# Optimization experiments

Hardware: AMD Instinct MI355X
Metric: run time of the kernel (lower is better)

The kernel has to match this reference:

```python
import jax, jax.numpy as jnp
import numpy as np
from jax import lax

# Fixed-point scales (powers of two, as in linger's luna/venus pipeline).
# scale_gi = input_scale * weight_ih_scale, scale_gh = hidden_scale * weight_hh_scale.
SCALE_GI = 2.0 ** 14
SCALE_GH = 2.0 ** 14
Q27 = 2.0 ** 27
Q15 = 2.0 ** 15
Q31 = 2.0 ** 31
INT32_MIN = -(2.0 ** 31)
INT32_MAX = 2.0 ** 31 - 1


def quant_round(x, scale):
    # QuantMode.floor_add: floor(x*scale + 0.5)/scale, with straight-through gradient
    # (linger QAT rounding uses STE).
    q = jnp.floor(x * scale + 0.5) / scale
    return x + lax.stop_gradient(q - x)


@jax.custom_vjp
def qsigmoid(x):
    # Quantize input to Q27 int32, evaluate sigmoid, output Q31 -> requant to Q15.
    i_q27 = jnp.clip(jnp.floor(x * Q27 + 0.5), INT32_MIN, INT32_MAX)
    s = jax.nn.sigmoid(i_q27 / Q27)
    out_q31 = jnp.floor(s * Q31 + 0.5)
    out_q15 = jnp.floor(out_q31 * (2.0 ** -16) + 0.5)  # luna_requant(31 -> 15)
    return out_q15 / Q15

def _qsig_fwd(x):
    return qsigmoid(x), x

def _qsig_bwd(x, g):
    s = jax.nn.sigmoid(x)
    return (g * s * (1.0 - s),)

qsigmoid.defvjp(_qsig_fwd, _qsig_bwd)


@jax.custom_vjp
def qtanh(x):
    i_q27 = jnp.clip(jnp.floor(x * Q27 + 0.5), INT32_MIN, INT32_MAX)
    t = jnp.tanh(i_q27 / Q27)
    out_q31 = jnp.floor(t * Q31 + 0.5)
    out_q15 = jnp.floor(out_q31 * (2.0 ** -16) + 0.5)
    return out_q15 / Q15

def _qtanh_fwd(x):
    return qtanh(x), x

def _qtanh_bwd(x, g):
    t = jnp.tanh(x)
    return (g * (1.0 - t * t),)

qtanh.defvjp(_qtanh_fwd, _qtanh_bwd)


def setup_inputs() -> dict:
    key = jax.random.key(0)
    k = jax.random.split(key, 6)
    B, I, H = 8192, 512, 512
    return {
        "input_x": jax.random.normal(k[0], (B, I), dtype=jnp.float32),
        "hidden": jax.random.normal(k[1], (B, H), dtype=jnp.float32),
        "weight_ih": jax.random.normal(k[2], (3 * H, I), dtype=jnp.float32) * 0.05,
        "weight_hh": jax.random.normal(k[3], (3 * H, H), dtype=jnp.float32) * 0.05,
        "bias_ih": jax.random.normal(k[4], (3 * H,), dtype=jnp.float32) * 0.05,
        "bias_hh": jax.random.normal(k[5], (3 * H,), dtype=jnp.float32) * 0.05,
    }


def reference(input_x, hidden, weight_ih, weight_hh, bias_ih, bias_hh):
    # Dense gate projections: [B, 3H]
    gi = input_x @ weight_ih.T + bias_ih
    gh = hidden @ weight_hh.T + bias_hh
    # Requant gate pre-activations to fixed-point grid (biasih/biashh quantizers)
    gi = quant_round(gi, SCALE_GI)
    gh = quant_round(gh, SCALE_GH)
    i_r, i_i, i_n = jnp.split(gi, 3, axis=1)
    h_r, h_i, h_n = jnp.split(gh, 3, axis=1)
    resetgate = qsigmoid(i_r + h_r)
    inputgate = qsigmoid(i_i + h_i)
    # h_n requantized to Q27, reset*h_n product requantized to Q15
    h_n = quant_round(h_n, Q27)
    resetgate_h_n = quant_round(resetgate * h_n, Q15)
    newgate = qtanh(resetgate_h_n + i_n)
    new_hidden = quant_round(hidden, Q15)
    hy = newgate + inputgate * (new_hidden - newgate)
    return hy
```

## Files before the change

kernel.cpp:

```cpp
#include <hip/hip_runtime.h>
#include <math.h>


typedef _Float16 f16x8  __attribute__((ext_vector_type(8)));
typedef _Float16 f16x4  __attribute__((ext_vector_type(4)));
typedef __bf16   bf16x8 __attribute__((ext_vector_type(8)));
typedef float    f32x16 __attribute__((ext_vector_type(16)));

namespace {

constexpr int Bsz = 8192, Ksz = 512, Hsz = 512;
constexpr int BM = 64, BN = 64;

constexpr unsigned WCH0    = 16384u;
constexpr unsigned NCHUNK  = 16384u + 3072u;
constexpr unsigned WS_F16  = NCHUNK * 512u;
constexpr size_t   WS_NEED = (size_t)WS_F16 * 2;

__device__ __forceinline__ float qround(float x, float s, float invs) {
    return floorf(x * s + 0.5f) * invs;
}

__device__ __forceinline__ float qsigmoid_dev(float x) {
    float iq = floorf(x * 134217728.0f + 0.5f);
    iq = fminf(fmaxf(iq, -2147483648.0f), 2147483648.0f);
    float e = __expf(-iq * 7.450580596923828125e-9f);
    float s = __builtin_amdgcn_rcpf(1.0f + e);
    float q31 = floorf(s * 2147483648.0f + 0.5f);
    float q15 = floorf(q31 * 1.52587890625e-5f + 0.5f);
    return q15 * 3.0517578125e-5f;
}

__device__ __forceinline__ float qtanh_dev(float x) {
    float iq = floorf(x * 134217728.0f + 0.5f);
    iq = fminf(fmaxf(iq, -2147483648.0f), 2147483648.0f);
    float z = iq * 7.450580596923828125e-9f;
    float e = __expf(2.0f * z);
    float t = 1.0f - 2.0f * __builtin_amdgcn_rcpf(e + 1.0f);
    float q31 = floorf(t * 2147483648.0f + 0.5f);
    float q15 = floorf(q31 * 1.52587890625e-5f + 0.5f);
    return q15 * 3.0517578125e-5f;
}

__device__ __forceinline__ void dma16(const void* g, void* l) {
    __builtin_amdgcn_global_load_lds(
        (const __attribute__((address_space(1))) unsigned int*)g,
        (__attribute__((address_space(3))) unsigned int*)l, 16, 0, 0);
}

__device__ __forceinline__ void split2(float a, float b, unsigned& hi, unsigned& lo) {
    unsigned ua = __float_as_uint(a); ua += 0x7fffu + ((ua >> 16) & 1u);
    unsigned ub = __float_as_uint(b); ub += 0x7fffu + ((ub >> 16) & 1u);
    hi = (ua >> 16) | (ub & 0xffff0000u);
    float ra = a - __uint_as_float(ua & 0xffff0000u);
    float rb = b - __uint_as_float(ub & 0xffff0000u);
    unsigned va = __float_as_uint(ra); va += 0x7fffu + ((va >> 16) & 1u);
    unsigned vb = __float_as_uint(rb); vb += 0x7fffu + ((vb >> 16) & 1u);
    lo = (va >> 16) | (vb & 0xffff0000u);
}

}

__global__ __launch_bounds__(256) void cvt_lds_f16(
    const float* __restrict__ x, const float* __restrict__ h,
    const float* __restrict__ wih, const float* __restrict__ whh,
    _Float16* __restrict__ ws)
{
    __shared__ __align__(16) _Float16 lt[16384];

    const int b   = blockIdx.x;
    const int tid = threadIdx.x;

    const float* src;
    unsigned chbase;
    if (b < 512) {
        const int arr = b >> 8, M32 = b & 255;
        src = (arr ? h : x) + (size_t)M32 * 32u * 512u;
        chbase = (unsigned)arr * 8192u + (unsigned)M32 * 32u;
    } else {
        const int w = b - 512;
        const int g = w >> 4, N32 = w & 15;
        const int rowLocal = (g % 3) * 512 + N32 * 32;
        src = (g < 3 ? wih : whh) + (size_t)rowLocal * 512u;
        chbase = WCH0 + (unsigned)((g * 16 + N32) * 32);
    }

#pragma unroll
    for (int rep = 0; rep < 16; ++rep) {
        const int idx = rep * 256 + tid;
        const int row = idx >> 7;
        const int q   = idx & 127;
        const float4 v = *(const float4*)(src + (size_t)row * 512 + q * 4);
        const int K16  = q >> 2;
        const int kh   = (q >> 1) & 1;
        const int half = (q & 1) * 4;
        const int s    = q >> 1;
        const int rsw  = (row + s) & 31;
        f16x4 o;
        o[0] = (_Float16)v.x; o[1] = (_Float16)v.y;
        o[2] = (_Float16)v.z; o[3] = (_Float16)v.w;
        *(f16x4*)&lt[K16 * 512 + kh * 256 + rsw * 8 + half] = o;
    }
    __syncthreads();

    const int wid = tid >> 6, lane = tid & 63;
    const int kh  = lane >> 5, row = lane & 31;
#pragma unroll
    for (int cc = 0; cc < 8; ++cc) {
        const int K16 = wid * 8 + cc;
        const int rsw = (row + 2 * K16 + kh) & 31;
        const f16x8 o = *(const f16x8*)&lt[K16 * 512 + kh * 256 + rsw * 8];
        *(f16x8*)(ws + (size_t)(chbase + K16) * 512u + lane * 8) = o;
    }
}

__global__ __launch_bounds__(256, 2) void qgru_f16_dma2(
    const _Float16* __restrict__ ws, const float* __restrict__ hid,
    const float* __restrict__ bih, const float* __restrict__ bhh,
    float* __restrict__ out)
{
    __shared__ __align__(16) _Float16 lds[32768];

    const int t = threadIdx.x, lane = t & 63, wid = t >> 6;
    const int mt = wid >> 1, nt = wid & 1;
    const int m0 = blockIdx.x * BM, n0 = blockIdx.y * BN;

    unsigned goff[8];
    int      ldst[8];
    if (wid == 0) {
#pragma unroll
        for (int c = 0; c < 8; ++c) {
            int arr = c >> 2, mtc = (c >> 1) & 1, ks2 = c & 1;
            unsigned ch = (unsigned)arr * 8192u
                        + (unsigned)((m0 >> 5) + mtc) * 32u + (unsigned)ks2;
            goff[c] = ch * 1024u + (unsigned)lane * 16u;
            ldst[c] = (arr * 2 + mtc) * 1024 + ks2 * 512;
        }
    } else {
#pragma unroll
        for (int c = 0; c < 8; ++c) {
            int g = (wid - 1) * 2 + (c >> 2), ntc = (c >> 1) & 1, ks2 = c & 1;
            unsigned ch = WCH0
                        + (unsigned)((g * 16 + (n0 >> 5) + ntc) * 32) + (unsigned)ks2;
            goff[c] = ch * 1024u + (unsigned)lane * 16u;
            ldst[c] = 4096 + (g * 2 + ntc) * 1024 + ks2 * 512;
        }
    }

    f32x16 acc[6];
#pragma unroll
    for (int g = 0; g < 6; ++g)
#pragma unroll
        for (int i = 0; i < 16; ++i) acc[g][i] = 0.0f;

    const char* wsb = (const char*)ws;
    const int lr = lane & 31, lk8 = (lane >> 5) * 8;

#pragma unroll
    for (int c = 0; c < 8; ++c)
        dma16(wsb + goff[c], &lds[ldst[c]]);

    for (int step = 0; step < 16; ++step) {
        __syncthreads();

        if (step + 1 < 16) {
            const unsigned kb = (unsigned)(step + 1) * 2048u;
            const int nb = ((step + 1) & 1) * 16384;
#pragma unroll
            for (int c = 0; c < 8; ++c)
                dma16(wsb + goff[c] + kb, &lds[nb + ldst[c]]);
        }

        const int cb = (step & 1) * 16384;
#pragma unroll
        for (int ks2 = 0; ks2 < 2; ++ks2) {
            const int lfo = cb + ks2 * 512 + lk8 * 32 + lr * 8;
            const f16x8 ax = *(const f16x8*)&lds[lfo + (0 + mt) * 1024];
            const f16x8 ah = *(const f16x8*)&lds[lfo + (2 + mt) * 1024];
#pragma unroll
            for (int g = 0; g < 6; ++g) {
                const f16x8 b = *(const f16x8*)&lds[lfo + 4096 + (g * 2 + nt) * 1024];
                acc[g] = __builtin_amdgcn_mfma_f32_32x32x16_f16(
                             g < 3 ? ax : ah, b, acc[g], 0, 0, 0);
            }
        }
    }

    constexpr float S14 = 16384.0f,     I14 = 1.0f / 16384.0f;
    constexpr float S15 = 32768.0f,     I15 = 1.0f / 32768.0f;
    constexpr float S27 = 134217728.0f, I27 = 1.0f / 134217728.0f;

    const int lh = lane >> 5, l32 = lane & 31;
    const int n = n0 + nt * 32 + l32;
    const float br = bih[n], bi = bih[n + 512], bn = bih[n + 1024];
    const float cr = bhh[n], ci = bhh[n + 512], cn = bhh[n + 1024];

#pragma unroll
    for (int r = 0; r < 16; ++r) {
        const int row = (r & 3) + 8 * (r >> 2) + 4 * lh;
        const int m   = m0 + mt * 32 + row;
        const float hv = hid[(size_t)m * Hsz + n];

        float gir = qround(acc[0][r] + br, S14, I14);
        float gii = qround(acc[1][r] + bi, S14, I14);
        float gin = qround(acc[2][r] + bn, S14, I14);
        float ghr = qround(acc[3][r] + cr, S14, I14);
        float ghi = qround(acc[4][r] + ci, S14, I14);
        float ghn = qround(acc[5][r] + cn, S14, I14);
        float resetg = qsigmoid_dev(gir + ghr);
        float inputg = qsigmoid_dev(gii + ghi);
        float hn  = qround(ghn, S27, I27);
        float rh  = qround(resetg * hn, S15, I15);
        float newg = qtanh_dev(rh + gin);
        float nh  = qround(hv, S15, I15);
        out[(size_t)m * Hsz + n] = newg + inputg * (nh - newg);
    }
}

__global__ __launch_bounds__(256, 2) void qgru_mfma_bf16x3(
    const float* __restrict__ x, const float* __restrict__ hid,
    const float* __restrict__ wih, const float* __restrict__ whh,
    const float* __restrict__ bih, const float* __restrict__ bhh,
    float* __restrict__ out)
{
    __shared__ __align__(16) unsigned short lds[16384];

    const int t = threadIdx.x, lane = t & 63, wid = t >> 6;
    const int mt = wid >> 1, nt = wid & 1;
    const int m0 = blockIdx.x * BM, n0 = blockIdx.y * BN;
    const int s_r = t >> 2, s_k = (t & 3) << 2;
    const int s_kh = s_k >> 3, s_j = s_k & 7, s_rt = s_r >> 5, s_r32 = s_r & 31;

    const float* gA[2];
    gA[0] = x   + (size_t)(m0 + s_r) * Ksz + s_k;
    gA[1] = hid + (size_t)(m0 + s_r) * Ksz + s_k;
    const float* gW[6];
#pragma unroll
    for (int g = 0; g < 3; ++g) {
        gW[g]     = wih + (size_t)(g * Hsz + n0 + s_r) * Ksz + s_k;
        gW[g + 3] = whh + (size_t)(g * Hsz + n0 + s_r) * Ksz + s_k;
    }
    const int lh = lane >> 5, l32 = lane & 31;

    f32x16 acc[6];
#pragma unroll
    for (int g = 0; g < 6; ++g)
#pragma unroll
        for (int i = 0; i < 16; ++i) acc[g][i] = 0.0f;

    float4 vA[2], vW[6];
#pragma unroll
    for (int tt = 0; tt < 2; ++tt) vA[tt] = *(const float4*)gA[tt];
#pragma unroll
    for (int g = 0; g < 6; ++g)    vW[g]  = *(const float4*)gW[g];

    for (int k0 = 0; k0 < Ksz; k0 += 16) {
        __syncthreads();
#pragma unroll
        for (int tt = 0; tt < 2; ++tt) {
            unsigned h0, h1, l0, l1;
            split2(vA[tt].x, vA[tt].y, h0, l0);
            split2(vA[tt].z, vA[tt].w, h1, l1);
            unsigned bH = ((((tt*2+0)*2+s_rt)*2+s_kh)*32+s_r32)*8 + s_j;
            unsigned bL = ((((tt*2+1)*2+s_rt)*2+s_kh)*32+s_r32)*8 + s_j;
            *reinterpret_cast<uint2*>(&lds[bH]) = make_uint2(h0, h1);
            *reinterpret_cast<uint2*>(&lds[bL]) = make_uint2(l0, l1);
        }
#pragma unroll
        for (int g = 0; g < 6; ++g) {
            unsigned h0, h1, l0, l1;
            split2(vW[g].x, vW[g].y, h0, l0);
            split2(vW[g].z, vW[g].w, h1, l1);
            unsigned bH = 4096u + ((((g*2+0)*2+s_rt)*2+s_kh)*32+s_r32)*8 + s_j;
            unsigned bL = 4096u + ((((g*2+1)*2+s_rt)*2+s_kh)*32+s_r32)*8 + s_j;
            *reinterpret_cast<uint2*>(&lds[bH]) = make_uint2(h0, h1);
            *reinterpret_cast<uint2*>(&lds[bL]) = make_uint2(l0, l1);
        }
        __syncthreads();
        const int kn = (k0 + 16 < Ksz) ? (k0 + 16) : 0;
#pragma unroll
        for (int tt = 0; tt < 2; ++tt) vA[tt] = *(const float4*)(gA[tt] + kn);
#pragma unroll
        for (int g = 0; g < 6; ++g)    vW[g]  = *(const float4*)(gW[g] + kn);

        const bf16x8 ax_hi = *reinterpret_cast<const bf16x8*>(&lds[((((0)*2+mt)*2+lh)*32+l32)*8]);
        const bf16x8 ax_lo = *reinterpret_cast<const bf16x8*>(&lds[((((1)*2+mt)*2+lh)*32+l32)*8]);
        const bf16x8 ah_hi = *reinterpret_cast<const bf16x8*>(&lds[((((2)*2+mt)*2+lh)*32+l32)*8]);
        const bf16x8 ah_lo = *reinterpret_cast<const bf16x8*>(&lds[((((3)*2+mt)*2+lh)*32+l32)*8]);
#pragma unroll
        for (int g = 0; g < 6; ++g) {
            const bf16x8 b_hi = *reinterpret_cast<const bf16x8*>(&lds[4096u + ((((g*2+0)*2+nt)*2+lh)*32+l32)*8]);
            const bf16x8 b_lo = *reinterpret_cast<const bf16x8*>(&lds[4096u + ((((g*2+1)*2+nt)*2+lh)*32+l32)*8]);
            const bf16x8 a_hi = (g < 3) ? ax_hi : ah_hi;
            const bf16x8 a_lo = (g < 3) ? ax_lo : ah_lo;
            acc[g] = __builtin_amdgcn_mfma_f32_32x32x16_bf16(a_hi, b_hi, acc[g], 0, 0, 0);
            acc[g] = __builtin_amdgcn_mfma_f32_32x32x16_bf16(a_hi, b_lo, acc[g], 0, 0, 0);
            acc[g] = __builtin_amdgcn_mfma_f32_32x32x16_bf16(a_lo, b_hi, acc[g], 0, 0, 0);
        }
    }

    constexpr float S14 = 16384.0f,     I14 = 1.0f / 16384.0f;
    constexpr float S15 = 32768.0f,     I15 = 1.0f / 32768.0f;
    constexpr float S27 = 134217728.0f, I27 = 1.0f / 134217728.0f;
    const int n = n0 + nt * 32 + l32;
    const float br = bih[n], bi = bih[n + 512], bn = bih[n + 1024];
    const float cr = bhh[n], ci = bhh[n + 512], cn = bhh[n + 1024];
#pragma unroll
    for (int r = 0; r < 16; ++r) {
        const int row = (r & 3) + 8 * (r >> 2) + 4 * lh;
        const int m   = m0 + mt * 32 + row;
        const float hv = hid[(size_t)m * Hsz + n];
        float gir = qround(acc[0][r] + br, S14, I14);
        float gii = qround(acc[1][r] + bi, S14, I14);
        float gin = qround(acc[2][r] + bn, S14, I14);
        float ghr = qround(acc[3][r] + cr, S14, I14);
        float ghi = qround(acc[4][r] + ci, S14, I14);
        float ghn = qround(acc[5][r] + cn, S14, I14);
        float resetg = qsigmoid_dev(gir + ghr);
        float inputg = qsigmoid_dev(gii + ghi);
        float hn  = qround(ghn, S27, I27);
        float rh  = qround(resetg * hn, S15, I15);
        float newg = qtanh_dev(rh + gin);
        float nh  = qround(hv, S15, I15);
        out[(size_t)m * Hsz + n] = newg + inputg * (nh - newg);
    }
}

extern "C" void kernel_launch(void* const* d_in, const int* in_sizes, int n_in,
                              void* d_out, int out_size, void* d_ws, size_t ws_size,
                              hipStream_t stream) {
    const float* x   = (const float*)d_in[0];
    const float* hid = (const float*)d_in[1];
    const float* wih = (const float*)d_in[2];
    const float* whh = (const float*)d_in[3];
    const float* bih = (const float*)d_in[4];
    const float* bhh = (const float*)d_in[5];
    float* out = (float*)d_out;
    dim3 grid(Bsz / BM, Hsz / BN);

    if (ws_size >= WS_NEED) {
        cvt_lds_f16<<<512 + 96, 256, 0, stream>>>(
            x, hid, wih, whh, (_Float16*)d_ws);
        qgru_f16_dma2<<<grid, dim3(256), 0, stream>>>(
            (const _Float16*)d_ws, hid, bih, bhh, out);
    } else {
        qgru_mfma_bf16x3<<<grid, dim3(256), 0, stream>>>(
            x, hid, wih, whh, bih, bhh, out);
    }
}
```

Baseline: 131.0 us.

## Fuse activation fp32-to-f16 conversion into GEMM, pre-convert only weights

The prepass now converts only the weight matrices to swizzled f16 chunks, so x and hidden are no longer converted and written to the workspace. The GEMM kernel loads x and hidden as fp32 straight from global memory into registers and converts them per MFMA fragment, and the LDS double buffer holds only weight tiles. Less LDS per block allows three blocks per CU instead of two. The cost is that the activation loads are uncoalesced per-lane global reads with no LDS staging or prefetch, which could stall the MFMA loop, and each activation row is re-read by every N-tile block.

```diff
diff --git a/kernel.cpp b/kernel.cpp
--- a/kernel.cpp
+++ b/kernel.cpp
@@ -12,10 +12,8 @@
 constexpr int Bsz = 8192, Ksz = 512, Hsz = 512;
 constexpr int BM = 64, BN = 64;
 
-constexpr unsigned WCH0    = 16384u;
-constexpr unsigned NCHUNK  = 16384u + 3072u;
-constexpr unsigned WS_F16  = NCHUNK * 512u;
-constexpr size_t   WS_NEED = (size_t)WS_F16 * 2;
+constexpr unsigned NCHW    = 3072u;
+constexpr size_t   WS_NEED = (size_t)NCHW * 512u * 2u;
 
 __device__ __forceinline__ float qround(float x, float s, float invs) {
     return floorf(x * s + 0.5f) * invs;
@@ -48,6 +46,15 @@
         (__attribute__((address_space(3))) unsigned int*)l, 16, 0, 0);
 }
 
+__device__ __forceinline__ f16x8 cvt8(float4 a, float4 b) {
+    f16x8 r;
+    r[0] = (_Float16)a.x; r[1] = (_Float16)a.y;
+    r[2] = (_Float16)a.z; r[3] = (_Float16)a.w;
+    r[4] = (_Float16)b.x; r[5] = (_Float16)b.y;
+    r[6] = (_Float16)b.z; r[7] = (_Float16)b.w;
+    return r;
+}
+
 __device__ __forceinline__ void split2(float a, float b, unsigned& hi, unsigned& lo) {
     unsigned ua = __float_as_uint(a); ua += 0x7fffu + ((ua >> 16) & 1u);
     unsigned ub = __float_as_uint(b); ub += 0x7fffu + ((ub >> 16) & 1u);
@@ -61,8 +68,7 @@
 
 }
 
-__global__ __launch_bounds__(256) void cvt_lds_f16(
-    const float* __restrict__ x, const float* __restrict__ h,
+__global__ __launch_bounds__(256) void wcvt_f16(
     const float* __restrict__ wih, const float* __restrict__ whh,
     _Float16* __restrict__ ws)
 {
@@ -70,20 +76,10 @@
 
     const int b   = blockIdx.x;
     const int tid = threadIdx.x;
-
-    const float* src;
-    unsigned chbase;
-    if (b < 512) {
-        const int arr = b >> 8, M32 = b & 255;
-        src = (arr ? h : x) + (size_t)M32 * 32u * 512u;
-        chbase = (unsigned)arr * 8192u + (unsigned)M32 * 32u;
-    } else {
-        const int w = b - 512;
-        const int g = w >> 4, N32 = w & 15;
-        const int rowLocal = (g % 3) * 512 + N32 * 32;
-        src = (g < 3 ? wih : whh) + (size_t)rowLocal * 512u;
-        chbase = WCH0 + (unsigned)((g * 16 + N32) * 32);
-    }
+    const int g   = b >> 4, N32 = b & 15;
+    const int rowLocal = (g % 3) * 512 + N32 * 32;
+    const float* src = (g < 3 ? wih : whh) + (size_t)rowLocal * 512u;
+    const unsigned chbase = (unsigned)((g * 16 + N32) * 32);
 
 #pragma unroll
     for (int rep = 0; rep < 16; ++rep) {
@@ -94,8 +90,7 @@
         const int K16  = q >> 2;
         const int kh   = (q >> 1) & 1;
         const int half = (q & 1) * 4;
-        const int s    = q >> 1;
-        const int rsw  = (row + s) & 31;
+        const int rsw  = (row + (q >> 1)) & 31;
         f16x4 o;
         o[0] = (_Float16)v.x; o[1] = (_Float16)v.y;
         o[2] = (_Float16)v.z; o[3] = (_Float16)v.w;
@@ -114,38 +109,33 @@
     }
 }
 
-__global__ __launch_bounds__(256, 2) void qgru_f16_dma2(
-    const _Float16* __restrict__ ws, const float* __restrict__ hid,
+__global__ __launch_bounds__(256, 3) void qgru_fused_f16(
+    const float* __restrict__ x, const float* __restrict__ hid,
+    const _Float16* __restrict__ ws,
     const float* __restrict__ bih, const float* __restrict__ bhh,
     float* __restrict__ out)
 {
-    __shared__ __align__(16) _Float16 lds[32768];
+    __shared__ __align__(16) _Float16 lds[24576];
 
     const int t = threadIdx.x, lane = t & 63, wid = t >> 6;
     const int mt = wid >> 1, nt = wid & 1;
     const int m0 = blockIdx.x * BM, n0 = blockIdx.y * BN;
 
-    unsigned goff[8];
-    int      ldst[8];
-    if (wid == 0) {
-#pragma unroll
-        for (int c = 0; c < 8; ++c) {
-            int arr = c >> 2, mtc = (c >> 1) & 1, ks2 = c & 1;
-            unsigned ch = (unsigned)arr * 8192u
-                        + (unsigned)((m0 >> 5) + mtc) * 32u + (unsigned)ks2;
-            goff[c] = ch * 1024u + (unsigned)lane * 16u;
-            ldst[c] = (arr * 2 + mtc) * 1024 + ks2 * 512;
-        }
-    } else {
-#pragma unroll
-        for (int c = 0; c < 8; ++c) {
-            int g = (wid - 1) * 2 + (c >> 2), ntc = (c >> 1) & 1, ks2 = c & 1;
-            unsigned ch = WCH0
-                        + (unsigned)((g * 16 + (n0 >> 5) + ntc) * 32) + (unsigned)ks2;
-            goff[c] = ch * 1024u + (unsigned)lane * 16u;
-            ldst[c] = 4096 + (g * 2 + ntc) * 1024 + ks2 * 512;
-        }
-    }
+    unsigned goff[6];
+    int      ldst[6];
+#pragma unroll
+    for (int c = 0; c < 6; ++c) {
+        const int q = wid * 6 + c;
+        const int g = q >> 2, ntc = (q >> 1) & 1, ks2 = q & 1;
+        const unsigned ch = (unsigned)((g * 16 + (n0 >> 5) + ntc) * 32) + (unsigned)ks2;
+        goff[c] = ch * 1024u + (unsigned)lane * 16u;
+        ldst[c] = ((g * 2 + ntc) * 2 + ks2) * 512;
+    }
+
+    const int arow = m0 + mt * 32 + (lane & 31);
+    const int koff = (lane >> 5) * 8;
+    const float* pax = x   + (size_t)arow * Ksz + koff;
+    const float* pah = hid + (size_t)arow * Ksz + koff;
 
     f32x16 acc[6];
 #pragma unroll
@@ -154,10 +144,10 @@
         for (int i = 0; i < 16; ++i) acc[g][i] = 0.0f;
 
     const char* wsb = (const char*)ws;
-    const int lr = lane & 31, lk8 = (lane >> 5) * 8;
-
-#pragma unroll
-    for (int c = 0; c < 8; ++c)
+    const int lfo = (lane >> 5) * 256 + (lane & 31) * 8;
+
+#pragma unroll
+    for (int c = 0; c < 6; ++c)
         dma16(wsb + goff[c], &lds[ldst[c]]);
 
     for (int step = 0; step < 16; ++step) {
@@ -165,21 +155,26 @@
 
         if (step + 1 < 16) {
             const unsigned kb = (unsigned)(step + 1) * 2048u;
-            const int nb = ((step + 1) & 1) * 16384;
-#pragma unroll
-            for (int c = 0; c < 8; ++c)
+            const int nb = ((step + 1) & 1) * 12288;
+#pragma unroll
+            for (int c = 0; c < 6; ++c)
                 dma16(wsb + goff[c] + kb, &lds[nb + ldst[c]]);
         }
 
-        const int cb = (step & 1) * 16384;
+        const int cb = (step & 1) * 12288;
+        const int kbase = step * 32;
 #pragma unroll
         for (int ks2 = 0; ks2 < 2; ++ks2) {
-            const int lfo = cb + ks2 * 512 + lk8 * 32 + lr * 8;
-            const f16x8 ax = *(const f16x8*)&lds[lfo + (0 + mt) * 1024];
-            const f16x8 ah = *(const f16x8*)&lds[lfo + (2 + mt) * 1024];
+            const int ke = kbase + ks2 * 16;
+            const float4 a0 = *(const float4*)(pax + ke);
+            const float4 a1 = *(const float4*)(pax + ke + 4);
+            const float4 h0 = *(const float4*)(pah + ke);
+            const float4 h1 = *(const float4*)(pah + ke + 4);
+            const f16x8 ax = cvt8(a0, a1);
+            const f16x8 ah = cvt8(h0, h1);
 #pragma unroll
             for (int g = 0; g < 6; ++g) {
-                const f16x8 b = *(const f16x8*)&lds[lfo + 4096 + (g * 2 + nt) * 1024];
+                const f16x8 b = *(const f16x8*)&lds[cb + ((g * 2 + nt) * 2 + ks2) * 512 + lfo];
                 acc[g] = __builtin_amdgcn_mfma_f32_32x32x16_f16(
                              g < 3 ? ax : ah, b, acc[g], 0, 0, 0);
             }
@@ -339,10 +334,9 @@
     dim3 grid(Bsz / BM, Hsz / BN);
 
     if (ws_size >= WS_NEED) {
-        cvt_lds_f16<<<512 + 96, 256, 0, stream>>>(
-            x, hid, wih, whh, (_Float16*)d_ws);
-        qgru_f16_dma2<<<grid, dim3(256), 0, stream>>>(
-            (const _Float16*)d_ws, hid, bih, bhh, out);
+        wcvt_f16<<<96, 256, 0, stream>>>(wih, whh, (_Float16*)d_ws);
+        qgru_fused_f16<<<grid, dim3(256), 0, stream>>>(
+            x, hid, (const _Float16*)d_ws, bih, bhh, out);
     } else {
         qgru_mfma_bf16x3<<<grid, dim3(256), 0, stream>>>(
             x, hid, wih, whh, bih, bhh, out);
```

After: 178.4 us. +36.1%, slower.
